# Performance work log

Hardware: AMD Instinct MI355X
Metric: run time of the kernel (lower is better)

The kernel has to match this reference:

```python
import jax, jax.numpy as jnp
import numpy as np
import math

N_H = 16

def _rope(x):
    # x: [b, h, n, d_k]; standard RoPE with half-split rotation
    n, d_k = x.shape[2], x.shape[3]
    inv_freq = 1.0 / (10000.0 ** (jnp.arange(0, d_k, 2, dtype=jnp.float32) / d_k))  # [d_k/2]
    freqs = jnp.arange(n, dtype=jnp.float32)[:, None] * inv_freq[None, :]            # [n, d_k/2]
    cos = jnp.concatenate([jnp.cos(freqs), jnp.cos(freqs)], axis=-1)[None, None]     # [1,1,n,d_k]
    sin = jnp.concatenate([jnp.sin(freqs), jnp.sin(freqs)], axis=-1)[None, None]
    x1, x2 = jnp.split(x, 2, axis=-1)
    rot = jnp.concatenate([-x2, x1], axis=-1)
    return x * cos + rot * sin


def setup_inputs() -> dict:
    key = jax.random.key(0)
    k1, k2, k3, k4 = jax.random.split(key, 4)
    b, n, d_m = 2, 1024, 2048
    x = jax.random.normal(k1, (b, n, d_m), dtype=jnp.float32)
    # causal mask (1 = keep, 0 = masked)
    m = jnp.tril(jnp.ones((n, n), dtype=jnp.int32))[None, None]  # [1,1,n,n]
    s = 1.0 / math.sqrt(d_m)
    Wqkv = jax.random.normal(k2, (d_m, 3 * d_m), dtype=jnp.float32) * s
    Wout = jax.random.normal(k3, (d_m, d_m), dtype=jnp.float32) * s
    bout = jax.random.normal(k4, (d_m,), dtype=jnp.float32) * 0.01
    return {"x": x, "m": m, "Wqkv": Wqkv, "Wout": Wout, "bout": bout}


def reference(x, m, Wqkv, Wout, bout):
    b, n, d = x.shape
    d_k = d // N_H
    qkv = (x @ Wqkv).reshape(b, n, 3, N_H, d_k)
    qkv = jnp.transpose(qkv, (2, 0, 3, 1, 4))  # [3, b, h, n, d_k]
    q, k, v = qkv[0], qkv[1], qkv[2]
    q, k = _rope(q), _rope(k)
    s = jnp.einsum('bhqd,bhkd->bhqk', q, k) / math.sqrt(d_k)
    s = jnp.where(m == 0, -jnp.inf, s)
    a = jax.nn.softmax(s, axis=-1)  # dropout is identity in eval / drop=0
    r = jnp.einsum('bhqk,bhkd->bhqd', a, v)
    r = jnp.transpose(r, (0, 2, 1, 3)).reshape(b, n, d)
    return r @ Wout + bout
```

## Files before the change

kernel.cpp:

```cpp
#include <hip/hip_runtime.h>
#include <math.h>

typedef unsigned short u16;
typedef unsigned int u32;
typedef __attribute__((ext_vector_type(8))) short short8;
typedef __attribute__((ext_vector_type(4))) float f32x4;

#define DEVI __device__ __forceinline__

DEVI u16 f2bf(float x) {
    union { float f; u32 u; } un; un.f = x;
    u32 u = un.u;
    return (u16)((u + 0x7fffu + ((u >> 16) & 1u)) >> 16);
}
DEVI float bf2f(u16 v) {
    union { u32 u; float f; } un; un.u = ((u32)v) << 16;
    return un.f;
}
DEVI f32x4 mfma_bf16(short8 a, short8 b, f32x4 c) {
    return __builtin_amdgcn_mfma_f32_16x16x32_bf16(a, b, c, 0, 0, 0);
}
DEVI void gload_lds16(const void* g, void* l) {
    __builtin_amdgcn_global_load_lds((const __attribute__((address_space(1))) u32*)g,
                                     (__attribute__((address_space(3))) u32*)l,
                                     16, 0, 0);
}

__global__ void k_convert_bf16(const float* __restrict__ in, u16* __restrict__ out, long n) {
    long idx = ((long)blockIdx.x * 256 + threadIdx.x) * 4;
    if (idx >= n) return;
    float4 v = *(const float4*)(in + idx);
    ushort4 o;
    o.x = f2bf(v.x); o.y = f2bf(v.y); o.z = f2bf(v.z); o.w = f2bf(v.w);
    *(ushort4*)(out + idx) = o;
}

__global__ void k_transpose_f32_bf16(const float* __restrict__ in, u16* __restrict__ out,
                                     int R, int C) {
    __shared__ u16 tile[64][68];
    const int tx = threadIdx.x & 15, ty = threadIdx.x >> 4;
    const long r0 = (long)blockIdx.y * 64, c0 = (long)blockIdx.x * 64;
#pragma unroll
    for (int p = 0; p < 4; ++p) {
        int r = ty + p * 16;
        float4 v = *(const float4*)(in + (r0 + r) * C + c0 + tx * 4);
        ushort4 o;
        o.x = f2bf(v.x); o.y = f2bf(v.y); o.z = f2bf(v.z); o.w = f2bf(v.w);
        *(ushort4*)&tile[r][tx * 4] = o;
    }
    __syncthreads();
#pragma unroll
    for (int p = 0; p < 4; ++p) {
        int rr = ty + p * 16;
        ushort4 o;
        o.x = tile[tx * 4 + 0][rr];
        o.y = tile[tx * 4 + 1][rr];
        o.z = tile[tx * 4 + 2][rr];
        o.w = tile[tx * 4 + 3][rr];
        *(ushort4*)(out + (c0 + rr) * R + r0 + tx * 4) = o;
    }
}

__global__ void k_transpose_v(const u16* __restrict__ in, u16* __restrict__ out) {
    __shared__ u16 tile[64][68];
    const int tx = threadIdx.x & 15, ty = threadIdx.x >> 4;
    const int bh = blockIdx.z;
    const long ib = (long)bh * 1024 * 128;
    const long ob = (long)bh * 128 * 1024;
    const int r0 = blockIdx.y * 64, c0 = blockIdx.x * 64;
#pragma unroll
    for (int p = 0; p < 4; ++p) {
        int r = ty + p * 16;
        ushort4 v = *(const ushort4*)(in + ib + (long)(r0 + r) * 128 + c0 + tx * 4);
        *(ushort4*)&tile[r][tx * 4] = v;
    }
    __syncthreads();
#pragma unroll
    for (int p = 0; p < 4; ++p) {
        int rr = ty + p * 16;
        ushort4 o;
        o.x = tile[tx * 4 + 0][rr];
        o.y = tile[tx * 4 + 1][rr];
        o.z = tile[tx * 4 + 2][rr];
        o.w = tile[tx * 4 + 3][rr];
        *(ushort4*)(out + ob + (long)(c0 + rr) * 1024 + r0 + tx * 4) = o;
    }
}

__global__ void k_rope(u16* __restrict__ q, u16* __restrict__ k) {
    const int idx = blockIdx.x * 256 + threadIdx.x;
    const int i = idx & 63;
    const int pos = (idx >> 6) & 1023;
    const int bh = idx >> 16;
    const long base = ((long)bh * 1024 + pos) * 128;
    float inv = exp2f(-(float)i * 0.20762050593045952f);
    float theta = (float)pos * inv;
    float sv, cv;
    sincosf(theta, &sv, &cv);
    {
        float x1 = bf2f(q[base + i]), x2 = bf2f(q[base + i + 64]);
        q[base + i]      = f2bf(x1 * cv - x2 * sv);
        q[base + i + 64] = f2bf(x2 * cv + x1 * sv);
    }
    {
        float x1 = bf2f(k[base + i]), x2 = bf2f(k[base + i + 64]);
        k[base + i]      = f2bf(x1 * cv - x2 * sv);
        k[base + i + 64] = f2bf(x2 * cv + x1 * sv);
    }
}

template <int EPI>
__global__ __launch_bounds__(256, 2) void k_gemm(const u16* __restrict__ A,
                                                 const u16* __restrict__ BT, int K,
                                                 u16* __restrict__ qb, u16* __restrict__ kb,
                                                 u16* __restrict__ vb, float* __restrict__ out,
                                                 const float* __restrict__ bias) {
    __shared__ u16 As[128 * 64];
    __shared__ u16 Bs[128 * 64];
    const int tid = threadIdx.x;
    const int lane = tid & 63, wave = tid >> 6;
    const int lm = lane & 15, quad = lane >> 4;
    const int wm = wave >> 1, wn = wave & 1;
    const int bm = blockIdx.x, bn = blockIdx.y;

    f32x4 acc[4][4] = {};

    const int srow = lane >> 3;
    const int scb = (lane & 7) ^ srow;
    const long arow0 = (long)bm * 128;
    const long brow0 = (long)bn * 128;

    for (int k0 = 0; k0 < K; k0 += 64) {
        __syncthreads();
#pragma unroll
        for (int it = 0; it < 4; ++it) {
            int ch = wave * 4 + it;
            long r = ch * 8 + srow;
            gload_lds16(A + (arow0 + r) * K + k0 + scb * 8, (char*)As + ch * 1024);
            gload_lds16(BT + (brow0 + r) * K + k0 + scb * 8, (char*)Bs + ch * 1024);
        }
        __syncthreads();
#pragma unroll
        for (int ko = 0; ko < 2; ++ko) {
            short8 af[4], bf[4];
#pragma unroll
            for (int i = 0; i < 4; ++i) {
                int row = wm * 64 + i * 16 + lm;
                int pc = (ko * 4 + quad) ^ (lm & 7);
                af[i] = *(const short8*)&As[row * 64 + pc * 8];
            }
#pragma unroll
            for (int j = 0; j < 4; ++j) {
                int row = wn * 64 + j * 16 + lm;
                int pc = (ko * 4 + quad) ^ (lm & 7);
                bf[j] = *(const short8*)&Bs[row * 64 + pc * 8];
            }
#pragma unroll
            for (int i = 0; i < 4; ++i)
#pragma unroll
                for (int j = 0; j < 4; ++j)
                    acc[i][j] = mfma_bf16(af[i], bf[j], acc[i][j]);
        }
    }

    if constexpr (EPI == 0) {
        const int which = bn >> 4;
        const int h = bn & 15;
        u16* dst = (which == 0) ? qb : ((which == 1) ? kb : vb);
        const int b = bm >> 3;
        const long hb = ((long)(b * 16 + h)) * 1024;
#pragma unroll
        for (int i = 0; i < 4; ++i) {
            const int row = bm * 128 + wm * 64 + i * 16 + quad * 4;
            const int pos = row & 1023;
#pragma unroll
            for (int r = 0; r < 4; ++r) {
#pragma unroll
                for (int j = 0; j < 4; ++j) {
                    const int dk = wn * 64 + j * 16 + lm;
                    dst[(hb + pos + r) * 128 + dk] = f2bf(acc[i][j][r]);
                }
            }
        }
    } else {
        float bv[4];
#pragma unroll
        for (int j = 0; j < 4; ++j) bv[j] = bias[bn * 128 + wn * 64 + j * 16 + lm];
#pragma unroll
        for (int i = 0; i < 4; ++i) {
#pragma unroll
            for (int r = 0; r < 4; ++r) {
                const int row = bm * 128 + wm * 64 + i * 16 + quad * 4 + r;
#pragma unroll
                for (int j = 0; j < 4; ++j) {
                    const int col = bn * 128 + wn * 64 + j * 16 + lm;
                    out[(long)row * 2048 + col] = acc[i][j][r] + bv[j];
                }
            }
        }
    }
}

__global__ __launch_bounds__(256, 2) void k_flash(const u16* __restrict__ Q,
                                                  const u16* __restrict__ Kb,
                                                  const u16* __restrict__ VT,
                                                  u16* __restrict__ R) {
    __shared__ u16 Ks[64 * 128];
    __shared__ u16 Vs[128 * 64];
    __shared__ u16 Ps[64 * 72];
    const int tid = threadIdx.x;
    const int lane = tid & 63, wave = tid >> 6;
    const int lm = lane & 15, quad = lane >> 4;
    const int id = blockIdx.x;
    const int g = id >> 8, rem = id & 255;
    const int bh = rem >> 3, s = rem & 7;
    const int qt = g ? (15 - s) : s;
    const long qkbase = (long)bh * 1024 * 128;
    const long vtbase = (long)bh * 128 * 1024;
    const int q0 = qt * 64;

    short8 qf[4];
    {
        const u16* qrow = Q + qkbase + (long)(q0 + wave * 16 + lm) * 128 + quad * 8;
#pragma unroll
        for (int kc = 0; kc < 4; ++kc) qf[kc] = *(const short8*)(qrow + kc * 32);
    }

    f32x4 o_acc[8] = {};
    float m_i = -INFINITY, l_i = 0.f;
    const float cl2e = 0.08838834764831845f * 1.4426950408889634f;

    const int kr = lane >> 4;
    const int kcb = (lane & 15) ^ kr;
    const int vr = lane >> 3;
    const int vcb = (lane & 7) ^ vr;

    for (int kt = 0; kt <= qt; ++kt) {
        __syncthreads();
        {
#pragma unroll
            for (int it = 0; it < 4; ++it) {
                int ch = wave * 4 + it;
                int krow = ch * 4 + kr;
                int kchunk = (lane & 15) ^ (krow & 15);
                gload_lds16(Kb + qkbase + (long)(kt * 64 + krow) * 128 + kchunk * 8,
                            (char*)Ks + ch * 1024);
                int vrow = ch * 8 + vr;
                gload_lds16(VT + vtbase + (long)vrow * 1024 + kt * 64 + vcb * 8,
                            (char*)Vs + ch * 1024);
            }
        }
        __syncthreads();

        f32x4 s_acc[4] = {};
#pragma unroll
        for (int kc = 0; kc < 4; ++kc) {
#pragma unroll
            for (int mi = 0; mi < 4; ++mi) {
                int row = mi * 16 + lm;
                int pc = (kc * 4 + quad) ^ lm;
                short8 ak = *(const short8*)&Ks[row * 128 + pc * 8];
                s_acc[mi] = mfma_bf16(ak, qf[kc], s_acc[mi]);
            }
        }
        const int qg = q0 + wave * 16 + lm;
        float t[4][4];
        float cmax = -INFINITY;
#pragma unroll
        for (int mi = 0; mi < 4; ++mi)
#pragma unroll
            for (int r = 0; r < 4; ++r) {
                int kg = kt * 64 + mi * 16 + quad * 4 + r;
                float val = (kg <= qg) ? s_acc[mi][r] * cl2e : -INFINITY;
                t[mi][r] = val;
                cmax = fmaxf(cmax, val);
            }
        cmax = fmaxf(cmax, __shfl_xor(cmax, 16));
        cmax = fmaxf(cmax, __shfl_xor(cmax, 32));
        float m_new = fmaxf(m_i, cmax);
        float alpha = exp2f(m_i - m_new);
        float csum = 0.f;
#pragma unroll
        for (int mi = 0; mi < 4; ++mi)
#pragma unroll
            for (int r = 0; r < 4; ++r) {
                float p = exp2f(t[mi][r] - m_new);
                t[mi][r] = p;
                csum += p;
            }
        csum += __shfl_xor(csum, 16);
        csum += __shfl_xor(csum, 32);
        l_i = l_i * alpha + csum;
        m_i = m_new;
#pragma unroll
        for (int mi = 0; mi < 4; ++mi) {
            ushort4 pk;
            pk.x = f2bf(t[mi][0]); pk.y = f2bf(t[mi][1]);
            pk.z = f2bf(t[mi][2]); pk.w = f2bf(t[mi][3]);
            *(ushort4*)&Ps[(wave * 16 + lm) * 72 + mi * 16 + quad * 4] = pk;
        }
        float aq[4];
#pragma unroll
        for (int r = 0; r < 4; ++r) aq[r] = __shfl(alpha, quad * 4 + r, 64);
#pragma unroll
        for (int nt = 0; nt < 8; ++nt)
#pragma unroll
            for (int r = 0; r < 4; ++r) o_acc[nt][r] *= aq[r];
#pragma unroll
        for (int kc = 0; kc < 2; ++kc) {
            short8 ap = *(const short8*)&Ps[(wave * 16 + lm) * 72 + kc * 32 + quad * 8];
#pragma unroll
            for (int nt = 0; nt < 8; ++nt) {
                int row = nt * 16 + lm;
                int pc = (kc * 4 + quad) ^ (lm & 7);
                short8 bv = *(const short8*)&Vs[row * 64 + pc * 8];
                o_acc[nt] = mfma_bf16(ap, bv, o_acc[nt]);
            }
        }
    }
    float lq[4];
#pragma unroll
    for (int r = 0; r < 4; ++r) lq[r] = __shfl(l_i, quad * 4 + r, 64);
    const int b = bh >> 4, h = bh & 15;
#pragma unroll
    for (int nt = 0; nt < 8; ++nt)
#pragma unroll
        for (int r = 0; r < 4; ++r) {
            const int pos = q0 + wave * 16 + quad * 4 + r;
            const int col = h * 128 + nt * 16 + lm;
            R[((long)b * 1024 + pos) * 2048 + col] = f2bf(o_acc[nt][r] / lq[r]);
        }
}

extern "C" void kernel_launch(void* const* d_in, const int* in_sizes, int n_in,
                              void* d_out, int out_size, void* d_ws, size_t ws_size,
                              hipStream_t stream) {
    const float* x    = (const float*)d_in[0];
    const float* Wqkv = (const float*)d_in[2];
    const float* Wout = (const float*)d_in[3];
    const float* bout = (const float*)d_in[4];
    float* out = (float*)d_out;

    char* ws = (char*)d_ws;
    u16* x_bf  = (u16*)(ws);
    u16* rbuf  = x_bf;
    u16* WqkvT = (u16*)(ws + (8L << 20));
    u16* vT    = WqkvT;
    u16* WoutT = (u16*)(ws + (32L << 20));
    u16* qbuf  = (u16*)(ws + (40L << 20));
    u16* kbuf  = (u16*)(ws + (48L << 20));
    u16* vbuf  = (u16*)(ws + (56L << 20));

    k_convert_bf16<<<4096, 256, 0, stream>>>(x, x_bf, 4194304);
    k_transpose_f32_bf16<<<dim3(96, 32), 256, 0, stream>>>(Wqkv, WqkvT, 2048, 6144);
    k_transpose_f32_bf16<<<dim3(32, 32), 256, 0, stream>>>(Wout, WoutT, 2048, 2048);
    k_gemm<0><<<dim3(16, 48), 256, 0, stream>>>(x_bf, WqkvT, 2048, qbuf, kbuf, vbuf,
                                                nullptr, nullptr);
    k_rope<<<8192, 256, 0, stream>>>(qbuf, kbuf);
    k_transpose_v<<<dim3(2, 16, 32), 256, 0, stream>>>(vbuf, vT);
    k_flash<<<512, 256, 0, stream>>>(qbuf, kbuf, vT, rbuf);
    k_gemm<1><<<dim3(16, 16), 256, 0, stream>>>(rbuf, WoutT, 2048, nullptr, nullptr, nullptr,
                                                out, bout);
}
```

Measured before the change: 259.1 us.

## Fuse RoPE and V transpose into QKV GEMM epilogue, merge prep kernels

The three input conversion and transpose kernels are merged into one prep kernel that picks its job from the block index. The QKV GEMM now stages its output tile in shared memory, a union that reuses the A/B tile space. From there it applies RoPE to Q and K with vectorized stores, or writes V already transposed. This drops the separate rope and V-transpose kernels, their extra round trips through global memory, and several launches. The cost is extra shared-memory traffic, an additional barrier, and sincos work inside the GEMM epilogue.

```diff
diff --git a/kernel.cpp b/kernel.cpp
--- a/kernel.cpp
+++ b/kernel.cpp
@@ -26,20 +26,33 @@
                                      16, 0, 0);
 }
 
-__global__ void k_convert_bf16(const float* __restrict__ in, u16* __restrict__ out, long n) {
-    long idx = ((long)blockIdx.x * 256 + threadIdx.x) * 4;
-    if (idx >= n) return;
-    float4 v = *(const float4*)(in + idx);
-    ushort4 o;
-    o.x = f2bf(v.x); o.y = f2bf(v.y); o.z = f2bf(v.z); o.w = f2bf(v.w);
-    *(ushort4*)(out + idx) = o;
-}
-
-__global__ void k_transpose_f32_bf16(const float* __restrict__ in, u16* __restrict__ out,
-                                     int R, int C) {
+__global__ void k_prep(const float* __restrict__ x, const float* __restrict__ Wqkv,
+                       const float* __restrict__ Wout, u16* __restrict__ x_bf,
+                       u16* __restrict__ WqkvT, u16* __restrict__ WoutT) {
     __shared__ u16 tile[64][68];
+    const int bid = blockIdx.x;
+    if (bid < 4096) {
+        long idx = ((long)bid * 256 + threadIdx.x) * 4;
+        float4 v = *(const float4*)(x + idx);
+        ushort4 o;
+        o.x = f2bf(v.x); o.y = f2bf(v.y); o.z = f2bf(v.z); o.w = f2bf(v.w);
+        *(ushort4*)(x_bf + idx) = o;
+        return;
+    }
+    const float* in;
+    u16* out;
+    int R, C, bx, by;
+    if (bid < 7168) {
+        int lb = bid - 4096;
+        in = Wqkv; out = WqkvT; R = 2048; C = 6144;
+        bx = lb % 96; by = lb / 96;
+    } else {
+        int lb = bid - 7168;
+        in = Wout; out = WoutT; R = 2048; C = 2048;
+        bx = lb & 31; by = lb >> 5;
+    }
     const int tx = threadIdx.x & 15, ty = threadIdx.x >> 4;
-    const long r0 = (long)blockIdx.y * 64, c0 = (long)blockIdx.x * 64;
+    const long r0 = (long)by * 64, c0 = (long)bx * 64;
 #pragma unroll
     for (int p = 0; p < 4; ++p) {
         int r = ty + p * 16;
@@ -61,62 +74,16 @@
     }
 }
 
-__global__ void k_transpose_v(const u16* __restrict__ in, u16* __restrict__ out) {
-    __shared__ u16 tile[64][68];
-    const int tx = threadIdx.x & 15, ty = threadIdx.x >> 4;
-    const int bh = blockIdx.z;
-    const long ib = (long)bh * 1024 * 128;
-    const long ob = (long)bh * 128 * 1024;
-    const int r0 = blockIdx.y * 64, c0 = blockIdx.x * 64;
-#pragma unroll
-    for (int p = 0; p < 4; ++p) {
-        int r = ty + p * 16;
-        ushort4 v = *(const ushort4*)(in + ib + (long)(r0 + r) * 128 + c0 + tx * 4);
-        *(ushort4*)&tile[r][tx * 4] = v;
-    }
-    __syncthreads();
-#pragma unroll
-    for (int p = 0; p < 4; ++p) {
-        int rr = ty + p * 16;
-        ushort4 o;
-        o.x = tile[tx * 4 + 0][rr];
-        o.y = tile[tx * 4 + 1][rr];
-        o.z = tile[tx * 4 + 2][rr];
-        o.w = tile[tx * 4 + 3][rr];
-        *(ushort4*)(out + ob + (long)(c0 + rr) * 1024 + r0 + tx * 4) = o;
-    }
-}
-
-__global__ void k_rope(u16* __restrict__ q, u16* __restrict__ k) {
-    const int idx = blockIdx.x * 256 + threadIdx.x;
-    const int i = idx & 63;
-    const int pos = (idx >> 6) & 1023;
-    const int bh = idx >> 16;
-    const long base = ((long)bh * 1024 + pos) * 128;
-    float inv = exp2f(-(float)i * 0.20762050593045952f);
-    float theta = (float)pos * inv;
-    float sv, cv;
-    sincosf(theta, &sv, &cv);
-    {
-        float x1 = bf2f(q[base + i]), x2 = bf2f(q[base + i + 64]);
-        q[base + i]      = f2bf(x1 * cv - x2 * sv);
-        q[base + i + 64] = f2bf(x2 * cv + x1 * sv);
-    }
-    {
-        float x1 = bf2f(k[base + i]), x2 = bf2f(k[base + i + 64]);
-        k[base + i]      = f2bf(x1 * cv - x2 * sv);
-        k[base + i + 64] = f2bf(x2 * cv + x1 * sv);
-    }
-}
-
 template <int EPI>
 __global__ __launch_bounds__(256, 2) void k_gemm(const u16* __restrict__ A,
                                                  const u16* __restrict__ BT, int K,
                                                  u16* __restrict__ qb, u16* __restrict__ kb,
-                                                 u16* __restrict__ vb, float* __restrict__ out,
+                                                 u16* __restrict__ vtb, float* __restrict__ out,
                                                  const float* __restrict__ bias) {
-    __shared__ u16 As[128 * 64];
-    __shared__ u16 Bs[128 * 64];
+    __shared__ union SM {
+        struct { u16 As[128 * 64]; u16 Bs[128 * 64]; } s;
+        u16 T[128 * 132];
+    } sm;
     const int tid = threadIdx.x;
     const int lane = tid & 63, wave = tid >> 6;
     const int lm = lane & 15, quad = lane >> 4;
@@ -136,8 +103,8 @@
         for (int it = 0; it < 4; ++it) {
             int ch = wave * 4 + it;
             long r = ch * 8 + srow;
-            gload_lds16(A + (arow0 + r) * K + k0 + scb * 8, (char*)As + ch * 1024);
-            gload_lds16(BT + (brow0 + r) * K + k0 + scb * 8, (char*)Bs + ch * 1024);
+            gload_lds16(A + (arow0 + r) * K + k0 + scb * 8, (char*)sm.s.As + ch * 1024);
+            gload_lds16(BT + (brow0 + r) * K + k0 + scb * 8, (char*)sm.s.Bs + ch * 1024);
         }
         __syncthreads();
 #pragma unroll
@@ -147,13 +114,13 @@
             for (int i = 0; i < 4; ++i) {
                 int row = wm * 64 + i * 16 + lm;
                 int pc = (ko * 4 + quad) ^ (lm & 7);
-                af[i] = *(const short8*)&As[row * 64 + pc * 8];
+                af[i] = *(const short8*)&sm.s.As[row * 64 + pc * 8];
             }
 #pragma unroll
             for (int j = 0; j < 4; ++j) {
                 int row = wn * 64 + j * 16 + lm;
                 int pc = (ko * 4 + quad) ^ (lm & 7);
-                bf[j] = *(const short8*)&Bs[row * 64 + pc * 8];
+                bf[j] = *(const short8*)&sm.s.Bs[row * 64 + pc * 8];
             }
 #pragma unroll
             for (int i = 0; i < 4; ++i)
@@ -164,22 +131,68 @@
     }
 
     if constexpr (EPI == 0) {
-        const int which = bn >> 4;
-        const int h = bn & 15;
-        u16* dst = (which == 0) ? qb : ((which == 1) ? kb : vb);
-        const int b = bm >> 3;
-        const long hb = ((long)(b * 16 + h)) * 1024;
-#pragma unroll
-        for (int i = 0; i < 4; ++i) {
-            const int row = bm * 128 + wm * 64 + i * 16 + quad * 4;
-            const int pos = row & 1023;
-#pragma unroll
-            for (int r = 0; r < 4; ++r) {
-#pragma unroll
-                for (int j = 0; j < 4; ++j) {
-                    const int dk = wn * 64 + j * 16 + lm;
-                    dst[(hb + pos + r) * 128 + dk] = f2bf(acc[i][j][r]);
+        __syncthreads();
+#pragma unroll
+        for (int i = 0; i < 4; ++i)
+#pragma unroll
+            for (int j = 0; j < 4; ++j) {
+                const int col = wn * 64 + j * 16 + lm;
+#pragma unroll
+                for (int r = 0; r < 4; ++r) {
+                    const int row = wm * 64 + i * 16 + quad * 4 + r;
+                    sm.T[row * 132 + col] = f2bf(acc[i][j][r]);
                 }
+            }
+        __syncthreads();
+        const int which = bn >> 4, h = bn & 15, b = bm >> 3;
+        const int p0 = (bm & 7) * 128;
+        if (which < 2) {
+            u16* dst = which ? kb : qb;
+            const long hb = ((long)(b * 16 + h)) * 1024;
+#pragma unroll
+            for (int c = 0; c < 8; ++c) {
+                const int lin = c * 1024 + tid * 4;
+                const int pos_l = lin >> 6;
+                const int i0 = lin & 63;
+                ushort4 cur = *(const ushort4*)&sm.T[pos_l * 132 + i0];
+                ushort4 par = *(const ushort4*)&sm.T[pos_l * 132 + i0 + 64];
+                const float pg = (float)(p0 + pos_l);
+                ushort4 o1, o2;
+                const u16* cp = (const u16*)&cur;
+                const u16* pp = (const u16*)&par;
+                u16* o1p = (u16*)&o1;
+                u16* o2p = (u16*)&o2;
+#pragma unroll
+                for (int e = 0; e < 4; ++e) {
+                    float inv = exp2f(-(float)(i0 + e) * 0.20762050593045952f);
+                    float sv, cv;
+                    sincosf(pg * inv, &sv, &cv);
+                    float x1 = bf2f(cp[e]), x2 = bf2f(pp[e]);
+                    o1p[e] = f2bf(x1 * cv - x2 * sv);
+                    o2p[e] = f2bf(x2 * cv + x1 * sv);
+                }
+                const long rowb = (hb + p0 + pos_l) * 128;
+                *(ushort4*)(dst + rowb + i0) = o1;
+                *(ushort4*)(dst + rowb + i0 + 64) = o2;
+            }
+        } else {
+            const long vrow = ((long)(b * 16 + h)) * 128;
+#pragma unroll
+            for (int c = 0; c < 8; ++c) {
+                const int lin = c * 2048 + tid * 8;
+                const int dk = lin >> 7;
+                const int ps = lin & 127;
+                ushort4 o1, o2;
+                u16* o1p = (u16*)&o1;
+                u16* o2p = (u16*)&o2;
+#pragma unroll
+                for (int e = 0; e < 4; ++e) {
+                    o1p[e] = sm.T[(ps + e) * 132 + dk];
+                    o2p[e] = sm.T[(ps + 4 + e) * 132 + dk];
+                }
+                u16* dst = vtb + (vrow + dk) * 1024 + p0 + ps;
+                *(ushort4*)dst = o1;
+                *(ushort4*)(dst + 4) = o2;
             }
         }
     } else {
@@ -231,7 +244,6 @@
     const float cl2e = 0.08838834764831845f * 1.4426950408889634f;
 
     const int kr = lane >> 4;
-    const int kcb = (lane & 15) ^ kr;
     const int vr = lane >> 3;
     const int vcb = (lane & 7) ^ vr;
 
@@ -345,20 +357,15 @@
     u16* x_bf  = (u16*)(ws);
     u16* rbuf  = x_bf;
     u16* WqkvT = (u16*)(ws + (8L << 20));
-    u16* vT    = WqkvT;
     u16* WoutT = (u16*)(ws + (32L << 20));
     u16* qbuf  = (u16*)(ws + (40L << 20));
     u16* kbuf  = (u16*)(ws + (48L << 20));
-    u16* vbuf  = (u16*)(ws + (56L << 20));
-
-    k_convert_bf16<<<4096, 256, 0, stream>>>(x, x_bf, 4194304);
-    k_transpose_f32_bf16<<<dim3(96, 32), 256, 0, stream>>>(Wqkv, WqkvT, 2048, 6144);
-    k_transpose_f32_bf16<<<dim3(32, 32), 256, 0, stream>>>(Wout, WoutT, 2048, 2048);
-    k_gemm<0><<<dim3(16, 48), 256, 0, stream>>>(x_bf, WqkvT, 2048, qbuf, kbuf, vbuf,
+    u16* vtbuf = (u16*)(ws + (56L << 20));
+
+    k_prep<<<8192, 256, 0, stream>>>(x, Wqkv, Wout, x_bf, WqkvT, WoutT);
+    k_gemm<0><<<dim3(16, 48), 256, 0, stream>>>(x_bf, WqkvT, 2048, qbuf, kbuf, vtbuf,
                                                 nullptr, nullptr);
-    k_rope<<<8192, 256, 0, stream>>>(qbuf, kbuf);
-    k_transpose_v<<<dim3(2, 16, 32), 256, 0, stream>>>(vbuf, vT);
-    k_flash<<<512, 256, 0, stream>>>(qbuf, kbuf, vT, rbuf);
+    k_flash<<<512, 256, 0, stream>>>(qbuf, kbuf, vtbuf, rbuf);
     k_gemm<1><<<dim3(16, 16), 256, 0, stream>>>(rbuf, WoutT, 2048, nullptr, nullptr, nullptr,
                                                 out, bout);
 }
```

Result: no change. 256.3 us (-1.1%).
